# Optimization experiments

Measured on AMD Instinct MI355X. Metric: run time of the kernel, lower is better.

## Reference

```python
import jax, jax.numpy as jnp
import numpy as np

H_DIM = 64      # input_dim of edge_aggregation (== h_dim)
HID = 128       # hidden_size of each per-edge-type agg MLP
T = 5           # edge_types for non-nba dataset
B, E, N = 64, 1024, 512


def setup_inputs() -> dict:
    key = jax.random.key(0)
    ks = jax.random.split(key, 8)
    edge_distribution = jax.random.uniform(ks[0], (B, E, T), dtype=jnp.float32)
    H = jax.random.uniform(ks[1], (B, E, N), dtype=jnp.float32)
    ori = jax.random.normal(ks[2], (B, N, H_DIM), dtype=jnp.float32)
    s1 = 1.0 / np.sqrt(H_DIM)
    s2 = 1.0 / np.sqrt(HID)
    # stacked per-edge-type MLP params: Linear(64->128) -> ReLU -> Linear(128->64)
    W1 = jax.random.uniform(ks[3], (T, H_DIM, HID), minval=-s1, maxval=s1, dtype=jnp.float32)
    b1 = jax.random.uniform(ks[4], (T, HID), minval=-s1, maxval=s1, dtype=jnp.float32)
    W2 = jax.random.uniform(ks[5], (T, HID, H_DIM), minval=-s2, maxval=s2, dtype=jnp.float32)
    b2 = jax.random.uniform(ks[6], (T, H_DIM), minval=-s2, maxval=s2, dtype=jnp.float32)
    return {"edge_distribution": edge_distribution, "H": H, "ori": ori,
            "W1": W1, "b1": b1, "W2": W2, "b2": b2}


def reference(edge_distribution, H, ori, W1, b1, W2, b2):
    # incidence gather: hyperedge features [B, E, D]
    edges = jnp.matmul(H, ori)
    # per-edge-type 2-layer MLP, vectorized over the T edge types
    h = jax.nn.relu(jnp.einsum('bed,tdh->bteh', edges, W1) + b1[None, :, None, :])
    per_type = jnp.einsum('bteh,thd->bted', h, W2) + b2[None, :, None, :]
    # mixture-weighted sum over edge types -> [B, E, D]
    edge_feature = jnp.einsum('bet,bted->bed', edge_distribution, per_type)
    # scatter back through H^T and concat with original node features
    node_agg = jnp.einsum('ben,bed->bnd', H, edge_feature)  # H^T @ edge_feature
    node_feature = jnp.concatenate((node_agg, ori), axis=-1)  # [B, N, 2D]
    return node_feature
```

## Files before the change

### kernel.cpp

```cpp
#include <hip/hip_runtime.h>

#define B_   64
#define E_   1024
#define N_   512
#define D_   64
#define HID_ 128
#define T_   5

typedef __bf16 bf16x8 __attribute__((ext_vector_type(8)));
typedef float f32x4 __attribute__((ext_vector_type(4)));

__device__ __forceinline__ unsigned short f2bu(float f) {
    union { float f; unsigned int u; } v; v.f = f;
    unsigned int r = (v.u + 0x7fffu + ((v.u >> 16) & 1u)) >> 16;
    return (unsigned short)r;
}

__device__ __forceinline__ unsigned int pack2(float lo, float hi) {
    union { __bf16 b[2]; unsigned int u; } v;
    v.b[0] = (__bf16)lo; v.b[1] = (__bf16)hi;
    return v.u;
}

__device__ __forceinline__ uint4 cvt8(float4 a, float4 b) {
    union { __bf16 h[8]; uint4 u; } v;
    v.h[0] = (__bf16)a.x; v.h[1] = (__bf16)a.y; v.h[2] = (__bf16)a.z; v.h[3] = (__bf16)a.w;
    v.h[4] = (__bf16)b.x; v.h[5] = (__bf16)b.y; v.h[6] = (__bf16)b.z; v.h[7] = (__bf16)b.w;
    return v.u;
}

#define MFMA16(a, b, c) __builtin_amdgcn_mfma_f32_16x16x32_bf16((a), (b), (c), 0, 0, 0)

__global__ __launch_bounds__(256) void k_prep_w(const float* __restrict__ W1,
                                                const float* __restrict__ W2,
                                                unsigned short* __restrict__ W1T,
                                                unsigned short* __restrict__ W2T) {
    int idx = blockIdx.x * 256 + threadIdx.x;
    if (idx < T_ * HID_ * D_) {
        int t = idx / (HID_ * D_), rem = idx % (HID_ * D_);
        int h = rem / D_, d = rem % D_;
        W1T[idx] = f2bu(W1[(t * D_ + d) * HID_ + h]);
    } else {
        int j = idx - T_ * HID_ * D_;
        int t = j / (D_ * HID_), rem = j % (D_ * HID_);
        int d = rem / HID_, h = rem % HID_;
        W2T[j] = f2bu(W2[(t * HID_ + h) * D_ + d]);
    }
}

__global__ __launch_bounds__(256) void k_ori_prep(const float* __restrict__ ori,
                                                  float* __restrict__ out,
                                                  unsigned short* __restrict__ oriT) {
    int b = blockIdx.y, n0 = blockIdx.x * 64;
    __shared__ float tl[64 * 65];
    int tid = threadIdx.x;
    int dl = tid & 63;
    #pragma unroll 4
    for (int p = 0; p < 16; ++p) {
        int nn = p * 4 + (tid >> 6);
        float v = ori[(size_t)(b * N_ + n0 + nn) * D_ + dl];
        out[(size_t)(b * N_ + n0 + nn) * 128 + 64 + dl] = v;
        tl[dl * 65 + nn] = v;
    }
    __syncthreads();
    #pragma unroll 4
    for (int p = 0; p < 16; ++p) {
        int dd = p * 4 + (tid >> 6);
        oriT[(size_t)(b * D_ + dd) * N_ + n0 + dl] = f2bu(tl[dd * 65 + dl]);
    }
}

__global__ __launch_bounds__(256) void k_edge_mlp(const float* __restrict__ H,
                                                  const unsigned short* __restrict__ oriT,
                                                  const float* __restrict__ ed,
                                                  const float* __restrict__ b1,
                                                  const float* __restrict__ b2,
                                                  const unsigned short* __restrict__ W1T,
                                                  const unsigned short* __restrict__ W2T,
                                                  unsigned short* __restrict__ efT) {
    int bx = blockIdx.x;
    int b = bx >> 4, e0 = (bx & 15) * 64;
    __shared__ __align__(16) unsigned short X[22528];
    __shared__ float wd_sh[320];
    __shared__ float b1_sh[640];
    __shared__ float b2_sh[320];
    int tid = threadIdx.x, w = tid >> 6, l = tid & 63, q = l >> 4, c = l & 15;
    int rs = tid >> 3, sgs = tid & 7;
    int swsl = (sgs ^ (rs & 7)) * 8;

    for (int u = tid; u < 320; u += 256) wd_sh[u] = ed[((size_t)b * E_ + e0) * T_ + u];
    for (int u = tid; u < 640; u += 256) b1_sh[u] = b1[u];
    for (int u = tid; u < 320; u += 256) b2_sh[u] = b2[u];

    const f32x4 zero = {0.f, 0.f, 0.f, 0.f};

    f32x4 acc1[4];
    #pragma unroll
    for (int fn = 0; fn < 4; ++fn) acc1[fn] = zero;

    const float* Hb = &H[((size_t)b * E_ + e0) * N_];
    const unsigned short* Ob = &oriT[(size_t)b * D_ * N_];

    float4 f00, f01, f10, f11;
    uint4 ob0, ob1;
    {
        const float* s0 = Hb + (size_t)rs * N_ + sgs * 8;
        const float* s1 = Hb + (size_t)(rs + 32) * N_ + sgs * 8;
        f00 = *(const float4*)&s0[0]; f01 = *(const float4*)&s0[4];
        f10 = *(const float4*)&s1[0]; f11 = *(const float4*)&s1[4];
        ob0 = *(const uint4*)&Ob[(size_t)rs * N_ + sgs * 8];
        ob1 = *(const uint4*)&Ob[(size_t)(rs + 32) * N_ + sgs * 8];
    }
    {
        unsigned short* aA = X;
        unsigned short* bB = X + 4096;
        *(uint4*)&aA[rs * 64 + swsl] = cvt8(f00, f01);
        *(uint4*)&aA[(rs + 32) * 64 + swsl] = cvt8(f10, f11);
        *(uint4*)&bB[rs * 64 + swsl] = ob0;
        *(uint4*)&bB[(rs + 32) * 64 + swsl] = ob1;
    }
    __syncthreads();

    for (int ks = 0; ks < 8; ++ks) {
        if (ks < 7) {
            int k0 = (ks + 1) * 64;
            const float* s0 = Hb + (size_t)rs * N_ + k0 + sgs * 8;
            const float* s1 = Hb + (size_t)(rs + 32) * N_ + k0 + sgs * 8;
            f00 = *(const float4*)&s0[0]; f01 = *(const float4*)&s0[4];
            f10 = *(const float4*)&s1[0]; f11 = *(const float4*)&s1[4];
            ob0 = *(const uint4*)&Ob[(size_t)rs * N_ + k0 + sgs * 8];
            ob1 = *(const uint4*)&Ob[(size_t)(rs + 32) * N_ + k0 + sgs * 8];
        }
        const unsigned short* aA = X + (ks & 1) * 8192;
        const unsigned short* bB = aA + 4096;
        #pragma unroll
        for (int hh = 0; hh < 2; ++hh) {
            int sl = ((hh * 4 + q) ^ (c & 7)) * 8;
            bf16x8 a0 = *(const bf16x8*)&aA[(w * 16 + c) * 64 + sl];
            #pragma unroll
            for (int fn = 0; fn < 4; ++fn) {
                bf16x8 bb = *(const bf16x8*)&bB[(fn * 16 + c) * 64 + sl];
                acc1[fn] = MFMA16(a0, bb, acc1[fn]);
            }
        }
        if (ks < 7) {
            unsigned short* aN = X + ((ks & 1) ^ 1) * 8192;
            unsigned short* bN = aN + 4096;
            *(uint4*)&aN[rs * 64 + swsl] = cvt8(f00, f01);
            *(uint4*)&aN[(rs + 32) * 64 + swsl] = cvt8(f10, f11);
            *(uint4*)&bN[rs * 64 + swsl] = ob0;
            *(uint4*)&bN[(rs + 32) * 64 + swsl] = ob1;
            __syncthreads();
        }
    }

    unsigned short* a_sh = X;
    unsigned short* w_sh = X + 4608;
    unsigned short* h_sh = X + 13824;
    #pragma unroll
    for (int fn = 0; fn < 4; ++fn)
        #pragma unroll
        for (int i = 0; i < 4; ++i)
            a_sh[(w * 16 + q * 4 + i) * 72 + fn * 16 + c] = f2bu(acc1[fn][i]);

    f32x4 y[4];
    #pragma unroll
    for (int fn = 0; fn < 4; ++fn) y[fn] = zero;

    #pragma unroll 1
    for (int t = 0; t < T_; ++t) {
        uint4 wr[4];
        #pragma unroll
        for (int p = 0; p < 4; ++p) {
            int u2 = p * 256 + tid;
            wr[p] = *(const uint4*)&W1T[((size_t)t * HID_ + (u2 >> 3)) * D_ + (u2 & 7) * 8];
        }
        __syncthreads();
        #pragma unroll
        for (int p = 0; p < 4; ++p) {
            int u2 = p * 256 + tid;
            *(uint4*)&w_sh[(u2 >> 3) * 72 + (u2 & 7) * 8] = wr[p];
        }
        __syncthreads();
        f32x4 hc[8];
        #pragma unroll
        for (int fn = 0; fn < 8; ++fn) hc[fn] = zero;
        #pragma unroll
        for (int ks = 0; ks < 2; ++ks) {
            bf16x8 a = *(const bf16x8*)&a_sh[(w * 16 + c) * 72 + ks * 32 + q * 8];
            #pragma unroll
            for (int fn = 0; fn < 8; ++fn) {
                bf16x8 bb = *(const bf16x8*)&w_sh[(fn * 16 + c) * 72 + ks * 32 + q * 8];
                hc[fn] = MFMA16(a, bb, hc[fn]);
            }
        }
        #pragma unroll
        for (int p = 0; p < 4; ++p) {
            int u2 = p * 256 + tid;
            wr[p] = *(const uint4*)&W2T[((size_t)t * D_ + (u2 >> 4)) * HID_ + (u2 & 15) * 8];
        }
        float wv[4];
        #pragma unroll
        for (int i = 0; i < 4; ++i) wv[i] = wd_sh[(w * 16 + q * 4 + i) * T_ + t];
        #pragma unroll
        for (int fn = 0; fn < 8; ++fn) {
            float b1v = b1_sh[t * HID_ + fn * 16 + c];
            #pragma unroll
            for (int i = 0; i < 4; ++i) {
                float v = hc[fn][i] + b1v;
                v = fmaxf(v, 0.0f) * wv[i];
                h_sh[(w * 16 + q * 4 + i) * 136 + fn * 16 + c] = f2bu(v);
            }
        }
        __syncthreads();
        #pragma unroll
        for (int p = 0; p < 4; ++p) {
            int u2 = p * 256 + tid;
            *(uint4*)&w_sh[(u2 >> 4) * 136 + (u2 & 15) * 8] = wr[p];
        }
        __syncthreads();
        #pragma unroll
        for (int ks = 0; ks < 4; ++ks) {
            bf16x8 a = *(const bf16x8*)&h_sh[(w * 16 + c) * 136 + ks * 32 + q * 8];
            #pragma unroll
            for (int fn = 0; fn < 4; ++fn) {
                bf16x8 bb = *(const bf16x8*)&w_sh[(fn * 16 + c) * 136 + ks * 32 + q * 8];
                y[fn] = MFMA16(a, bb, y[fn]);
            }
        }
    }
    #pragma unroll
    for (int fn = 0; fn < 4; ++fn) {
        int d = fn * 16 + c;
        ushort4 o;
        #pragma unroll
        for (int i = 0; i < 4; ++i) {
            int r = w * 16 + q * 4 + i;
            float s = y[fn][i];
            #pragma unroll
            for (int t = 0; t < T_; ++t) s += wd_sh[r * T_ + t] * b2_sh[t * D_ + d];
            ((unsigned short*)&o)[i] = f2bu(s);
        }
        *(ushort4*)&efT[((size_t)b * D_ + d) * E_ + e0 + w * 16 + q * 4] = o;
    }
}

__global__ __launch_bounds__(256) void k_gemm_out(const float* __restrict__ H,
                                                  const unsigned short* __restrict__ efT,
                                                  float* __restrict__ out) {
    int bid = blockIdx.x;
    int swz = (bid & 7) * 64 + (bid >> 3);
    int b = swz >> 3, n0 = (swz & 7) * 64;
    __shared__ __align__(16) unsigned short aA[2][64 * 72];
    __shared__ unsigned int bB32[2][64 * 33];
    int tid = threadIdx.x, w = tid >> 6, l = tid & 63, q = l >> 4, c = l & 15;
    int r2 = tid >> 3, cg = tid & 7;
    const f32x4 zero = {0.f, 0.f, 0.f, 0.f};
    f32x4 acc[4];
    #pragma unroll
    for (int fm = 0; fm < 4; ++fm) acc[fm] = zero;

    const unsigned short* Ab = &efT[(size_t)b * D_ * E_];
    const float* Hb = &H[(size_t)b * E_ * N_ + n0];

    uint4 ar0, ar1;
    float4 f0, f1, g0, g1;
    {
        ar0 = *(const uint4*)&Ab[(size_t)r2 * E_ + cg * 8];
        ar1 = *(const uint4*)&Ab[(size_t)(r2 + 32) * E_ + cg * 8];
        const float* s0 = Hb + (size_t)(2 * r2) * N_ + cg * 8;
        const float* s1 = s0 + N_;
        f0 = *(const float4*)&s0[0]; f1 = *(const float4*)&s0[4];
        g0 = *(const float4*)&s1[0]; g1 = *(const float4*)&s1[4];
    }
    {
        *(uint4*)&aA[0][r2 * 72 + cg * 8] = ar0;
        *(uint4*)&aA[0][(r2 + 32) * 72 + cg * 8] = ar1;
        float r0a[8] = {f0.x, f0.y, f0.z, f0.w, f1.x, f1.y, f1.z, f1.w};
        float r1a[8] = {g0.x, g0.y, g0.z, g0.w, g1.x, g1.y, g1.z, g1.w};
        #pragma unroll
        for (int j = 0; j < 8; ++j)
            bB32[0][(cg * 8 + j) * 33 + r2] = pack2(r0a[j], r1a[j]);
    }
    __syncthreads();

    for (int ks = 0; ks < 16; ++ks) {
        if (ks < 15) {
            int k0 = (ks + 1) * 64;
            ar0 = *(const uint4*)&Ab[(size_t)r2 * E_ + k0 + cg * 8];
            ar1 = *(const uint4*)&Ab[(size_t)(r2 + 32) * E_ + k0 + cg * 8];
            const float* s0 = Hb + (size_t)(k0 + 2 * r2) * N_ + cg * 8;
            const float* s1 = s0 + N_;
            f0 = *(const float4*)&s0[0]; f1 = *(const float4*)&s0[4];
            g0 = *(const float4*)&s1[0]; g1 = *(const float4*)&s1[4];
        }
        int cur = ks & 1;
        #pragma unroll
        for (int hh = 0; hh < 2; ++hh) {
            union { unsigned int u[4]; bf16x8 v; } bb;
            #pragma unroll
            for (int i = 0; i < 4; ++i)
                bb.u[i] = bB32[cur][(w * 16 + c) * 33 + hh * 16 + q * 4 + i];
            #pragma unroll
            for (int fm = 0; fm < 4; ++fm) {
                bf16x8 afr = *(const bf16x8*)&aA[cur][(fm * 16 + c) * 72 + hh * 32 + q * 8];
                acc[fm] = MFMA16(afr, bb.v, acc[fm]);
            }
        }
        if (ks < 15) {
            int nxt = cur ^ 1;
            *(uint4*)&aA[nxt][r2 * 72 + cg * 8] = ar0;
            *(uint4*)&aA[nxt][(r2 + 32) * 72 + cg * 8] = ar1;
            float r0a[8] = {f0.x, f0.y, f0.z, f0.w, f1.x, f1.y, f1.z, f1.w};
            float r1a[8] = {g0.x, g0.y, g0.z, g0.w, g1.x, g1.y, g1.z, g1.w};
            #pragma unroll
            for (int j = 0; j < 8; ++j)
                bB32[nxt][(cg * 8 + j) * 33 + r2] = pack2(r0a[j], r1a[j]);
            __syncthreads();
        }
    }
    #pragma unroll
    for (int fm = 0; fm < 4; ++fm) {
        *(f32x4*)&out[((size_t)b * N_ + n0 + w * 16 + c) * 128 + fm * 16 + q * 4] = acc[fm];
    }
}

extern "C" void kernel_launch(void* const* d_in, const int* in_sizes, int n_in,
                              void* d_out, int out_size, void* d_ws, size_t ws_size,
                              hipStream_t stream) {
    const float* ed  = (const float*)d_in[0];
    const float* H   = (const float*)d_in[1];
    const float* ori = (const float*)d_in[2];
    const float* W1  = (const float*)d_in[3];
    const float* b1  = (const float*)d_in[4];
    const float* W2  = (const float*)d_in[5];
    const float* b2  = (const float*)d_in[6];
    float* out = (float*)d_out;

    char* ws = (char*)d_ws;
    unsigned short* oriT = (unsigned short*)ws; ws += (size_t)B_ * D_ * N_ * 2;
    unsigned short* W1T  = (unsigned short*)ws; ws += (size_t)T_ * HID_ * D_ * 2;
    unsigned short* W2T  = (unsigned short*)ws; ws += (size_t)T_ * D_ * HID_ * 2;
    unsigned short* efT  = (unsigned short*)ws; ws += (size_t)B_ * D_ * E_ * 2;

    hipLaunchKernelGGL(k_prep_w, dim3(320), dim3(256), 0, stream, W1, W2, W1T, W2T);
    hipLaunchKernelGGL(k_ori_prep, dim3(8, 64), dim3(256), 0, stream, ori, out, oriT);
    hipLaunchKernelGGL(k_edge_mlp, dim3(1024), dim3(256), 0, stream,
                       H, oriT, ed, b1, b2, W1T, W2T, efT);
    hipLaunchKernelGGL(k_gemm_out, dim3(512), dim3(256), 0, stream, H, efT, out);
}
```

Baseline: 318.0 us.

## Cache bf16 copy of H in workspace for second GEMM, drop double buffering

```diff
diff --git a/kernel.cpp b/kernel.cpp
--- a/kernel.cpp
+++ b/kernel.cpp
@@ -77,10 +77,15 @@
                                                   const float* __restrict__ b2,
                                                   const unsigned short* __restrict__ W1T,
                                                   const unsigned short* __restrict__ W2T,
-                                                  unsigned short* __restrict__ efT) {
+                                                  unsigned short* __restrict__ efT,
+                                                  unsigned short* __restrict__ Hbf) {
     int bx = blockIdx.x;
     int b = bx >> 4, e0 = (bx & 15) * 64;
-    __shared__ __align__(16) unsigned short X[22528];
+    __shared__ __align__(16) unsigned short aA[64 * 64];
+    __shared__ __align__(16) unsigned short bB[64 * 64];
+    __shared__ __align__(16) unsigned short a_sh[64 * 72];
+    __shared__ __align__(16) unsigned short w_sh[128 * 72];
+    __shared__ __align__(16) unsigned short h_sh[64 * 136];
     __shared__ float wd_sh[320];
     __shared__ float b1_sh[640];
     __shared__ float b2_sh[320];
@@ -101,38 +106,24 @@
     const float* Hb = &H[((size_t)b * E_ + e0) * N_];
     const unsigned short* Ob = &oriT[(size_t)b * D_ * N_];
 
-    float4 f00, f01, f10, f11;
-    uint4 ob0, ob1;
-    {
-        const float* s0 = Hb + (size_t)rs * N_ + sgs * 8;
-        const float* s1 = Hb + (size_t)(rs + 32) * N_ + sgs * 8;
-        f00 = *(const float4*)&s0[0]; f01 = *(const float4*)&s0[4];
-        f10 = *(const float4*)&s1[0]; f11 = *(const float4*)&s1[4];
-        ob0 = *(const uint4*)&Ob[(size_t)rs * N_ + sgs * 8];
-        ob1 = *(const uint4*)&Ob[(size_t)(rs + 32) * N_ + sgs * 8];
-    }
-    {
-        unsigned short* aA = X;
-        unsigned short* bB = X + 4096;
-        *(uint4*)&aA[rs * 64 + swsl] = cvt8(f00, f01);
-        *(uint4*)&aA[(rs + 32) * 64 + swsl] = cvt8(f10, f11);
-        *(uint4*)&bB[rs * 64 + swsl] = ob0;
-        *(uint4*)&bB[(rs + 32) * 64 + swsl] = ob1;
-    }
-    __syncthreads();
-
     for (int ks = 0; ks < 8; ++ks) {
-        if (ks < 7) {
-            int k0 = (ks + 1) * 64;
-            const float* s0 = Hb + (size_t)rs * N_ + k0 + sgs * 8;
-            const float* s1 = Hb + (size_t)(rs + 32) * N_ + k0 + sgs * 8;
-            f00 = *(const float4*)&s0[0]; f01 = *(const float4*)&s0[4];
-            f10 = *(const float4*)&s1[0]; f11 = *(const float4*)&s1[4];
-            ob0 = *(const uint4*)&Ob[(size_t)rs * N_ + k0 + sgs * 8];
-            ob1 = *(const uint4*)&Ob[(size_t)(rs + 32) * N_ + k0 + sgs * 8];
-        }
-        const unsigned short* aA = X + (ks & 1) * 8192;
-        const unsigned short* bB = aA + 4096;
+        int k0 = ks * 64;
+        const float* s0 = Hb + (size_t)rs * N_ + k0 + sgs * 8;
+        const float* s1 = Hb + (size_t)(rs + 32) * N_ + k0 + sgs * 8;
+        float4 f00 = *(const float4*)&s0[0], f01 = *(const float4*)&s0[4];
+        float4 f10 = *(const float4*)&s1[0], f11 = *(const float4*)&s1[4];
+        uint4 ca = cvt8(f00, f01), cb = cvt8(f10, f11);
+        *(uint4*)&aA[rs * 64 + swsl] = ca;
+        *(uint4*)&aA[(rs + 32) * 64 + swsl] = cb;
+        *(uint4*)&bB[rs * 64 + swsl] =
+            *(const uint4*)&Ob[(size_t)rs * N_ + k0 + sgs * 8];
+        *(uint4*)&bB[(rs + 32) * 64 + swsl] =
+            *(const uint4*)&Ob[(size_t)(rs + 32) * N_ + k0 + sgs * 8];
+        if (Hbf) {
+            *(uint4*)&Hbf[((size_t)b * E_ + e0 + rs) * N_ + k0 + sgs * 8] = ca;
+            *(uint4*)&Hbf[((size_t)b * E_ + e0 + rs + 32) * N_ + k0 + sgs * 8] = cb;
+        }
+        __syncthreads();
         #pragma unroll
         for (int hh = 0; hh < 2; ++hh) {
             int sl = ((hh * 4 + q) ^ (c & 7)) * 8;
@@ -143,20 +134,8 @@
                 acc1[fn] = MFMA16(a0, bb, acc1[fn]);
             }
         }
-        if (ks < 7) {
-            unsigned short* aN = X + ((ks & 1) ^ 1) * 8192;
-            unsigned short* bN = aN + 4096;
-            *(uint4*)&aN[rs * 64 + swsl] = cvt8(f00, f01);
-            *(uint4*)&aN[(rs + 32) * 64 + swsl] = cvt8(f10, f11);
-            *(uint4*)&bN[rs * 64 + swsl] = ob0;
-            *(uint4*)&bN[(rs + 32) * 64 + swsl] = ob1;
-            __syncthreads();
-        }
-    }
-
-    unsigned short* a_sh = X;
-    unsigned short* w_sh = X + 4608;
-    unsigned short* h_sh = X + 13824;
+        __syncthreads();
+    }
     #pragma unroll
     for (int fn = 0; fn < 4; ++fn)
         #pragma unroll
@@ -167,19 +146,13 @@
     #pragma unroll
     for (int fn = 0; fn < 4; ++fn) y[fn] = zero;
 
-    #pragma unroll 1
     for (int t = 0; t < T_; ++t) {
-        uint4 wr[4];
+        __syncthreads();
         #pragma unroll
         for (int p = 0; p < 4; ++p) {
-            int u2 = p * 256 + tid;
-            wr[p] = *(const uint4*)&W1T[((size_t)t * HID_ + (u2 >> 3)) * D_ + (u2 & 7) * 8];
-        }
-        __syncthreads();
-        #pragma unroll
-        for (int p = 0; p < 4; ++p) {
-            int u2 = p * 256 + tid;
-            *(uint4*)&w_sh[(u2 >> 3) * 72 + (u2 & 7) * 8] = wr[p];
+            int u = p * 256 + tid, hh = u >> 3, sg = u & 7;
+            *(uint4*)&w_sh[hh * 72 + sg * 8] =
+                *(const uint4*)&W1T[(t * HID_ + hh) * D_ + sg * 8];
         }
         __syncthreads();
         f32x4 hc[8];
@@ -193,11 +166,6 @@
                 bf16x8 bb = *(const bf16x8*)&w_sh[(fn * 16 + c) * 72 + ks * 32 + q * 8];
                 hc[fn] = MFMA16(a, bb, hc[fn]);
             }
-        }
-        #pragma unroll
-        for (int p = 0; p < 4; ++p) {
-            int u2 = p * 256 + tid;
-            wr[p] = *(const uint4*)&W2T[((size_t)t * D_ + (u2 >> 4)) * HID_ + (u2 & 15) * 8];
         }
         float wv[4];
         #pragma unroll
@@ -215,8 +183,9 @@
         __syncthreads();
         #pragma unroll
         for (int p = 0; p < 4; ++p) {
-            int u2 = p * 256 + tid;
-            *(uint4*)&w_sh[(u2 >> 4) * 136 + (u2 & 15) * 8] = wr[p];
+            int u = p * 256 + tid, dd = u >> 4, sg = u & 15;
+            *(uint4*)&w_sh[dd * 136 + sg * 8] =
+                *(const uint4*)&W2T[(t * D_ + dd) * HID_ + sg * 8];
         }
         __syncthreads();
         #pragma unroll
@@ -246,6 +215,7 @@
 }
 
 __global__ __launch_bounds__(256) void k_gemm_out(const float* __restrict__ H,
+                                                  const unsigned short* __restrict__ Hbf,
                                                   const unsigned short* __restrict__ efT,
                                                   float* __restrict__ out) {
     int bid = blockIdx.x;
@@ -261,62 +231,115 @@
     for (int fm = 0; fm < 4; ++fm) acc[fm] = zero;
 
     const unsigned short* Ab = &efT[(size_t)b * D_ * E_];
-    const float* Hb = &H[(size_t)b * E_ * N_ + n0];
-
-    uint4 ar0, ar1;
-    float4 f0, f1, g0, g1;
-    {
-        ar0 = *(const uint4*)&Ab[(size_t)r2 * E_ + cg * 8];
-        ar1 = *(const uint4*)&Ab[(size_t)(r2 + 32) * E_ + cg * 8];
-        const float* s0 = Hb + (size_t)(2 * r2) * N_ + cg * 8;
-        const float* s1 = s0 + N_;
-        f0 = *(const float4*)&s0[0]; f1 = *(const float4*)&s0[4];
-        g0 = *(const float4*)&s1[0]; g1 = *(const float4*)&s1[4];
-    }
-    {
-        *(uint4*)&aA[0][r2 * 72 + cg * 8] = ar0;
-        *(uint4*)&aA[0][(r2 + 32) * 72 + cg * 8] = ar1;
-        float r0a[8] = {f0.x, f0.y, f0.z, f0.w, f1.x, f1.y, f1.z, f1.w};
-        float r1a[8] = {g0.x, g0.y, g0.z, g0.w, g1.x, g1.y, g1.z, g1.w};
-        #pragma unroll
-        for (int j = 0; j < 8; ++j)
-            bB32[0][(cg * 8 + j) * 33 + r2] = pack2(r0a[j], r1a[j]);
-    }
-    __syncthreads();
-
-    for (int ks = 0; ks < 16; ++ks) {
-        if (ks < 15) {
-            int k0 = (ks + 1) * 64;
-            ar0 = *(const uint4*)&Ab[(size_t)r2 * E_ + k0 + cg * 8];
-            ar1 = *(const uint4*)&Ab[(size_t)(r2 + 32) * E_ + k0 + cg * 8];
-            const float* s0 = Hb + (size_t)(k0 + 2 * r2) * N_ + cg * 8;
+
+    if (Hbf) {
+        const unsigned short* Hb2 = &Hbf[(size_t)b * E_ * N_ + n0];
+        union U8 { uint4 u; unsigned short s[8]; };
+        uint4 ar0, ar1;
+        U8 ha, hb;
+        {
+            ar0 = *(const uint4*)&Ab[(size_t)r2 * E_ + cg * 8];
+            ar1 = *(const uint4*)&Ab[(size_t)(r2 + 32) * E_ + cg * 8];
+            ha.u = *(const uint4*)&Hb2[(size_t)(2 * r2) * N_ + cg * 8];
+            hb.u = *(const uint4*)&Hb2[(size_t)(2 * r2 + 1) * N_ + cg * 8];
+        }
+        {
+            *(uint4*)&aA[0][r2 * 72 + cg * 8] = ar0;
+            *(uint4*)&aA[0][(r2 + 32) * 72 + cg * 8] = ar1;
+            #pragma unroll
+            for (int j = 0; j < 8; ++j)
+                bB32[0][(cg * 8 + j) * 33 + r2] =
+                    (unsigned int)ha.s[j] | ((unsigned int)hb.s[j] << 16);
+        }
+        __syncthreads();
+        for (int ks = 0; ks < 16; ++ks) {
+            if (ks < 15) {
+                int k0 = (ks + 1) * 64;
+                ar0 = *(const uint4*)&Ab[(size_t)r2 * E_ + k0 + cg * 8];
+                ar1 = *(const uint4*)&Ab[(size_t)(r2 + 32) * E_ + k0 + cg * 8];
+                ha.u = *(const uint4*)&Hb2[(size_t)(k0 + 2 * r2) * N_ + cg * 8];
+                hb.u = *(const uint4*)&Hb2[(size_t)(k0 + 2 * r2 + 1) * N_ + cg * 8];
+            }
+            int cur = ks & 1;
+            #pragma unroll
+            for (int hh = 0; hh < 2; ++hh) {
+                union { unsigned int u[4]; bf16x8 v; } bb;
+                #pragma unroll
+                for (int i = 0; i < 4; ++i)
+                    bb.u[i] = bB32[cur][(w * 16 + c) * 33 + hh * 16 + q * 4 + i];
+                #pragma unroll
+                for (int fm = 0; fm < 4; ++fm) {
+                    bf16x8 afr = *(const bf16x8*)&aA[cur][(fm * 16 + c) * 72 + hh * 32 + q * 8];
+                    acc[fm] = MFMA16(afr, bb.v, acc[fm]);
+                }
+            }
+            if (ks < 15) {
+                int nxt = cur ^ 1;
+                *(uint4*)&aA[nxt][r2 * 72 + cg * 8] = ar0;
+                *(uint4*)&aA[nxt][(r2 + 32) * 72 + cg * 8] = ar1;
+                #pragma unroll
+                for (int j = 0; j < 8; ++j)
+                    bB32[nxt][(cg * 8 + j) * 33 + r2] =
+                        (unsigned int)ha.s[j] | ((unsigned int)hb.s[j] << 16);
+                __syncthreads();
+            }
+        }
+    } else {
+        const float* Hb = &H[(size_t)b * E_ * N_ + n0];
+        uint4 ar0, ar1;
+        float4 f0, f1, g0, g1;
+        {
+            ar0 = *(const uint4*)&Ab[(size_t)r2 * E_ + cg * 8];
+            ar1 = *(const uint4*)&Ab[(size_t)(r2 + 32) * E_ + cg * 8];
+            const float* s0 = Hb + (size_t)(2 * r2) * N_ + cg * 8;
             const float* s1 = s0 + N_;
             f0 = *(const float4*)&s0[0]; f1 = *(const float4*)&s0[4];
             g0 = *(const float4*)&s1[0]; g1 = *(const float4*)&s1[4];
         }
-        int cur = ks & 1;
-        #pragma unroll
-        for (int hh = 0; hh < 2; ++hh) {
-            union { unsigned int u[4]; bf16x8 v; } bb;
-            #pragma unroll
-            for (int i = 0; i < 4; ++i)
-                bb.u[i] = bB32[cur][(w * 16 + c) * 33 + hh * 16 + q * 4 + i];
-            #pragma unroll
-            for (int fm = 0; fm < 4; ++fm) {
-                bf16x8 afr = *(const bf16x8*)&aA[cur][(fm * 16 + c) * 72 + hh * 32 + q * 8];
-                acc[fm] = MFMA16(afr, bb.v, acc[fm]);
-            }
-        }
-        if (ks < 15) {
-            int nxt = cur ^ 1;
-            *(uint4*)&aA[nxt][r2 * 72 + cg * 8] = ar0;
-            *(uint4*)&aA[nxt][(r2 + 32) * 72 + cg * 8] = ar1;
+        {
+            *(uint4*)&aA[0][r2 * 72 + cg * 8] = ar0;
+            *(uint4*)&aA[0][(r2 + 32) * 72 + cg * 8] = ar1;
             float r0a[8] = {f0.x, f0.y, f0.z, f0.w, f1.x, f1.y, f1.z, f1.w};
             float r1a[8] = {g0.x, g0.y, g0.z, g0.w, g1.x, g1.y, g1.z, g1.w};
             #pragma unroll
             for (int j = 0; j < 8; ++j)
-                bB32[nxt][(cg * 8 + j) * 33 + r2] = pack2(r0a[j], r1a[j]);
-            __syncthreads();
+                bB32[0][(cg * 8 + j) * 33 + r2] = pack2(r0a[j], r1a[j]);
+        }
+        __syncthreads();
+        for (int ks = 0; ks < 16; ++ks) {
+            if (ks < 15) {
+                int k0 = (ks + 1) * 64;
+                ar0 = *(const uint4*)&Ab[(size_t)r2 * E_ + k0 + cg * 8];
+                ar1 = *(const uint4*)&Ab[(size_t)(r2 + 32) * E_ + k0 + cg * 8];
+                const float* s0 = Hb + (size_t)(k0 + 2 * r2) * N_ + cg * 8;
+                const float* s1 = s0 + N_;
+                f0 = *(const float4*)&s0[0]; f1 = *(const float4*)&s0[4];
+                g0 = *(const float4*)&s1[0]; g1 = *(const float4*)&s1[4];
+            }
+            int cur = ks & 1;
+            #pragma unroll
+            for (int hh = 0; hh < 2; ++hh) {
+                union { unsigned int u[4]; bf16x8 v; } bb;
+                #pragma unroll
+                for (int i = 0; i < 4; ++i)
+                    bb.u[i] = bB32[cur][(w * 16 + c) * 33 + hh * 16 + q * 4 + i];
+                #pragma unroll
+                for (int fm = 0; fm < 4; ++fm) {
+                    bf16x8 afr = *(const bf16x8*)&aA[cur][(fm * 16 + c) * 72 + hh * 32 + q * 8];
+                    acc[fm] = MFMA16(afr, bb.v, acc[fm]);
+                }
+            }
+            if (ks < 15) {
+                int nxt = cur ^ 1;
+                *(uint4*)&aA[nxt][r2 * 72 + cg * 8] = ar0;
+                *(uint4*)&aA[nxt][(r2 + 32) * 72 + cg * 8] = ar1;
+                float r0a[8] = {f0.x, f0.y, f0.z, f0.w, f1.x, f1.y, f1.z, f1.w};
+                float r1a[8] = {g0.x, g0.y, g0.z, g0.w, g1.x, g1.y, g1.z, g1.w};
+                #pragma unroll
+                for (int j = 0; j < 8; ++j)
+                    bB32[nxt][(cg * 8 + j) * 33 + r2] = pack2(r0a[j], r1a[j]);
+                __syncthreads();
+            }
         }
     }
     #pragma unroll
@@ -338,14 +361,21 @@
     float* out = (float*)d_out;
 
     char* ws = (char*)d_ws;
-    unsigned short* oriT = (unsigned short*)ws; ws += (size_t)B_ * D_ * N_ * 2;
-    unsigned short* W1T  = (unsigned short*)ws; ws += (size_t)T_ * HID_ * D_ * 2;
-    unsigned short* W2T  = (unsigned short*)ws; ws += (size_t)T_ * D_ * HID_ * 2;
-    unsigned short* efT  = (unsigned short*)ws; ws += (size_t)B_ * D_ * E_ * 2;
+    size_t used = 0;
+    unsigned short* oriT = (unsigned short*)(ws + used); used += (size_t)B_ * D_ * N_ * 2;
+    unsigned short* W1T  = (unsigned short*)(ws + used); used += (size_t)T_ * HID_ * D_ * 2;
+    unsigned short* W2T  = (unsigned short*)(ws + used); used += (size_t)T_ * D_ * HID_ * 2;
+    unsigned short* efT  = (unsigned short*)(ws + used); used += (size_t)B_ * D_ * E_ * 2;
+    size_t hbf_bytes = (size_t)B_ * E_ * N_ * 2;
+    unsigned short* Hbf = nullptr;
+    if (ws_size >= used + hbf_bytes) {
+        Hbf = (unsigned short*)(ws + used);
+        used += hbf_bytes;
+    }
 
     hipLaunchKernelGGL(k_prep_w, dim3(320), dim3(256), 0, stream, W1, W2, W1T, W2T);
     hipLaunchKernelGGL(k_ori_prep, dim3(8, 64), dim3(256), 0, stream, ori, out, oriT);
     hipLaunchKernelGGL(k_edge_mlp, dim3(1024), dim3(256), 0, stream,
-                       H, oriT, ed, b1, b2, W1T, W2T, efT);
-    hipLaunchKernelGGL(k_gemm_out, dim3(512), dim3(256), 0, stream, H, efT, out);
-}
+                       H, oriT, ed, b1, b2, W1T, W2T, efT, Hbf);
+    hipLaunchKernelGGL(k_gemm_out, dim3(512), dim3(256), 0, stream, H, Hbf, efT, out);
+}
```

After: 274.2 us. 13.8% less time.
